# Kernel optimization log

Hardware: AMD Instinct MI355X
Metric: run time of the kernel (lower is better)

Reference implementation:

```python
import jax, jax.numpy as jnp
import numpy as np

DIM = 1024
HEADS = 16
EPS = 1e-05
B, T, C, H, W = 2, 16, DIM, 32, 32


def setup_inputs() -> dict:
    key = jax.random.key(0)
    ks = jax.random.split(key, 4)
    s = 1.0 / np.sqrt(DIM)
    return {
        "x": jax.random.normal(ks[0], (B, T, C, H, W), dtype=jnp.float32),
        "ln_w": jnp.ones((C,), dtype=jnp.float32),
        "ln_b": jnp.zeros((C,), dtype=jnp.float32),
        "Wq": jax.random.normal(ks[1], (C, C), dtype=jnp.float32) * s,
        "Wk": jax.random.normal(ks[2], (C, C), dtype=jnp.float32) * s,
        "Wv": jax.random.normal(ks[3], (C, C), dtype=jnp.float32) * s,
    }


def reference(x, ln_w, ln_b, Wq, Wk, Wv):
    b, t, c, h, w = x.shape
    heads = HEADS
    dh = c // heads
    scale = dh ** (-0.5)

    # Channel LayerNorm: normalize over C per (b,t,h,w)
    xc = jnp.transpose(x, (0, 1, 3, 4, 2))  # [B,T,H,W,C]
    mu = jnp.mean(xc, axis=-1, keepdims=True)
    var = jnp.mean(jnp.square(xc - mu), axis=-1, keepdims=True)
    xn = (xc - mu) * jax.lax.rsqrt(var + EPS) * ln_w + ln_b  # [B,T,H,W,C]

    # Q/K from spatial mean-pool
    pooled = jnp.mean(xn, axis=(2, 3))  # [B,T,C]
    q = pooled @ Wq.T  # [B,T,C]
    k = pooled @ Wk.T  # [B,T,C]

    # V per pixel; torch permutes to [B,W,H,T,C] then flattens W-major
    v = jnp.transpose(xn, (0, 3, 2, 1, 4)).reshape(b, h * w, t, c)  # [B,HW(w-major),T,C]
    v = v @ Wv.T

    q = q.reshape(b, t, heads, dh).transpose(0, 2, 1, 3) * scale  # [B,h,T,dh]
    k = k.reshape(b, t, heads, dh).transpose(0, 2, 3, 1)          # [B,h,dh,T]
    v = v.reshape(b, h * w, t, heads, dh).transpose(0, 1, 3, 2, 4)  # [B,HW,h,T,dh]

    attn = jax.nn.softmax(jnp.matmul(q, k), axis=-1)  # [B,h,T,T]
    out = jnp.einsum('bhst,bnhtd->bnhsd', attn, v)    # [B,HW,h,T,dh]
    # permute(0,3,2,4,1) -> [B,T,h,dh,HW], then view as (H,W)
    out = out.transpose(0, 3, 2, 4, 1).reshape(b, t, c, h, w)
    return out
```

## Files before the change

### kernel.cpp

```cpp
#include <hip/hip_runtime.h>
#include <stdint.h>
#include <stddef.h>

#define CDIM 1024
#define HWD  1024
#define TD   16
#define BD   2
#define NH   16
#define DHD  64

typedef __attribute__((ext_vector_type(8))) short bf16x8;
typedef __attribute__((ext_vector_type(4))) short bf16x4;
typedef __attribute__((ext_vector_type(4))) float f32x4;

static __device__ __forceinline__ short f2bf(float f) {
  uint32_t u = __builtin_bit_cast(uint32_t, f);
  uint32_t r = (u + 0x7FFFu + ((u >> 16) & 1u)) >> 16;
  return (short)(uint16_t)r;
}
static __device__ __forceinline__ float bf2f(short s) {
  return __builtin_bit_cast(float, (uint32_t)((uint16_t)s) << 16);
}

static __device__ __forceinline__ void gl_lds16(const short* g, short* l) {
  __builtin_amdgcn_global_load_lds((const __attribute__((address_space(1))) unsigned int*)g,
                                   (__attribute__((address_space(3))) unsigned int*)l,
                                   16, 0, 0);
}

__global__ void k_cast_w(const float* __restrict__ W, short* __restrict__ Wb) {
  int i = (blockIdx.x * 256 + threadIdx.x) * 4;
  f32x4 v = *(const f32x4*)&W[i];
  Wb[i + 0] = f2bf(v[0]);
  Wb[i + 1] = f2bf(v[1]);
  Wb[i + 2] = f2bf(v[2]);
  Wb[i + 3] = f2bf(v[3]);
}

__global__ __launch_bounds__(256) void k_ln_t(const float* __restrict__ x,
                                              const float* __restrict__ lnw,
                                              const float* __restrict__ lnb,
                                              short* __restrict__ xnT,
                                              float* __restrict__ part) {
  int bt = blockIdx.y;
  int p0 = blockIdx.x * 64;
  int tid = threadIdx.x;
  int pg = tid & 15, cs = tid >> 4;
  int pbase = p0 + pg * 4;
  const float* xs = x + (size_t)bt * CDIM * HWD;

  float s[4] = {}, s2[4] = {};
  #pragma unroll 8
  for (int j = 0; j < 64; ++j) {
    int c = cs + 16 * j;
    f32x4 v = *(const f32x4*)&xs[(size_t)c * HWD + pbase];
    #pragma unroll
    for (int i = 0; i < 4; ++i) { s[i] += v[i]; s2[i] += v[i] * v[i]; }
  }
  __shared__ float redA[16][64], redB[16][64];
  #pragma unroll
  for (int i = 0; i < 4; ++i) {
    redA[cs][pg * 4 + i] = s[i];
    redB[cs][pg * 4 + i] = s2[i];
  }
  __syncthreads();
  __shared__ float muS[64], rsS[64];
  if (tid < 64) {
    float a = 0.f, b2 = 0.f;
    #pragma unroll
    for (int k = 0; k < 16; ++k) { a += redA[k][tid]; b2 += redB[k][tid]; }
    float mu = a * (1.0f / CDIM);
    float var = b2 * (1.0f / CDIM) - mu * mu;
    muS[tid] = mu;
    rsS[tid] = rsqrtf(var + 1e-5f);
  }
  __syncthreads();
  float mu_[4], rs_[4];
  #pragma unroll
  for (int i = 0; i < 4; ++i) { mu_[i] = muS[pg * 4 + i]; rs_[i] = rsS[pg * 4 + i]; }

  __shared__ short tile[64 * 68];
  __shared__ float pr[64][17];
  short* outB = xnT + (size_t)bt * CDIM * HWD;

  for (int cb = 0; cb < 16; ++cb) {
    #pragma unroll
    for (int jj = 0; jj < 4; ++jj) {
      int cl = cs * 4 + jj;
      int c = cb * 64 + cl;
      f32x4 v = *(const f32x4*)&xs[(size_t)c * HWD + pbase];
      float w = lnw[c], bb = lnb[c];
      float psum = 0.f;
      #pragma unroll
      for (int i = 0; i < 4; ++i) {
        float xn = (v[i] - mu_[i]) * rs_[i] * w + bb;
        tile[(pg * 4 + i) * 68 + cl] = f2bf(xn);
        psum += xn;
      }
      pr[cl][pg] = psum;
    }
    __syncthreads();
    #pragma unroll
    for (int it = 0; it < 2; ++it) {
      int ch = it * 256 + tid;
      int plo = ch >> 3;
      int c8 = (ch & 7) * 8;
      bf16x4 a = *(const bf16x4*)&tile[plo * 68 + c8];
      bf16x4 b = *(const bf16x4*)&tile[plo * 68 + c8 + 4];
      int pq = p0 + plo;
      int q = (pq & 31) * 32 + (pq >> 5);
      short* dst = outB + (size_t)q * CDIM + cb * 64 + c8;
      *(bf16x4*)dst = a;
      *(bf16x4*)(dst + 4) = b;
    }
    if (tid < 64) {
      float a = 0.f;
      #pragma unroll
      for (int k = 0; k < 16; ++k) a += pr[tid][k];
      part[((size_t)bt * 16 + blockIdx.x) * CDIM + cb * 64 + tid] = a;
    }
    __syncthreads();
  }
}

__global__ void k_pool_red(const float* __restrict__ part, float* __restrict__ pooled,
                           short* __restrict__ pooledb) {
  int bt = blockIdx.y;
  int c = blockIdx.x * 256 + threadIdx.x;
  float s = 0.f;
  #pragma unroll
  for (int pc = 0; pc < 16; ++pc) s += part[((size_t)bt * 16 + pc) * CDIM + c];
  float m = s * (1.0f / HWD);
  pooled[bt * CDIM + c] = m;
  pooledb[bt * CDIM + c] = f2bf(m);
}

__global__ __launch_bounds__(256) void k_qk_mfma(const short* __restrict__ Wqkb,
                                                 const short* __restrict__ pooledb,
                                                 float* __restrict__ qm,
                                                 float* __restrict__ km) {
  int n0 = blockIdx.x * 128;
  __shared__ __align__(16) short lA[32 * 32];
  __shared__ __align__(16) short lB[128 * 32];
  int tid = threadIdx.x, lane = tid & 63, wid = tid >> 6;
  int s0 = wid * 128 + lane, s1 = s0 + 64;
  int fr = lane & 15, fk = (lane >> 4) * 8;
  f32x4 acc[2][2] = {};

  for (int kt = 0; kt < CDIM / 32; ++kt) {
    int k0 = kt * 32;
    __syncthreads();
    gl_lds16(&Wqkb[(size_t)(n0 + (s0 >> 2)) * CDIM + k0 + (s0 & 3) * 8], &lB[s0 * 8]);
    gl_lds16(&Wqkb[(size_t)(n0 + (s1 >> 2)) * CDIM + k0 + (s1 & 3) * 8], &lB[s1 * 8]);
    if (wid < 2) {
      gl_lds16(&pooledb[(size_t)(tid >> 2) * CDIM + k0 + (tid & 3) * 8], &lA[tid * 8]);
    }
    __syncthreads();
    bf16x8 af[2], bfr[2];
    #pragma unroll
    for (int mi = 0; mi < 2; ++mi)
      af[mi] = *(const bf16x8*)&lA[(mi * 16 + fr) * 32 + fk];
    #pragma unroll
    for (int ni = 0; ni < 2; ++ni)
      bfr[ni] = *(const bf16x8*)&lB[(wid * 32 + ni * 16 + fr) * 32 + fk];
    #pragma unroll
    for (int mi = 0; mi < 2; ++mi)
      #pragma unroll
      for (int ni = 0; ni < 2; ++ni)
        acc[mi][ni] = __builtin_amdgcn_mfma_f32_16x16x32_bf16(af[mi], bfr[ni], acc[mi][ni], 0, 0, 0);
  }

  int cr = lane >> 4;
  #pragma unroll
  for (int mi = 0; mi < 2; ++mi)
    #pragma unroll
    for (int ni = 0; ni < 2; ++ni)
      #pragma unroll
      for (int rr = 0; rr < 4; ++rr) {
        int row = mi * 16 + cr * 4 + rr;
        int col = n0 + wid * 32 + ni * 16 + fr;
        float v = acc[mi][ni][rr];
        if (col < 1024) qm[(size_t)row * CDIM + col] = v;
        else            km[(size_t)row * CDIM + col - 1024] = v;
      }
}

__global__ void k_attn(const float* __restrict__ qm, const float* __restrict__ km,
                       float* __restrict__ attn) {
  int bg = blockIdx.x;
  int b = bg >> 4, g = bg & 15;
  int s = threadIdx.x >> 4, t = threadIdx.x & 15;
  const float* qr = qm + (size_t)(b * TD + s) * CDIM + g * DHD;
  const float* kr = km + (size_t)(b * TD + t) * CDIM + g * DHD;
  float d = 0.f;
  #pragma unroll
  for (int i = 0; i < DHD; ++i) d += qr[i] * kr[i];
  d *= 0.125f;
  float m = d;
  #pragma unroll
  for (int off = 8; off; off >>= 1) m = fmaxf(m, __shfl_xor(m, off, 16));
  float e = __expf(d - m);
  float sum = e;
  #pragma unroll
  for (int off = 8; off; off >>= 1) sum += __shfl_xor(sum, off, 16);
  attn[(size_t)bg * 256 + s * 16 + t] = e / sum;
}

__global__ __launch_bounds__(512, 2) void k_vgemm(const short* __restrict__ Wb,
                                                  const short* __restrict__ xnT,
                                                  short* __restrict__ vp) {
  int bid = blockIdx.x;
  int swz = (bid & 7) * 64 + (bid >> 3);
  int bt = swz >> 4;
  int m0 = ((swz >> 2) & 3) * 256;
  int n0 = (swz & 3) * 256;
  const short* Bm = xnT + (size_t)bt * CDIM * HWD;

  __shared__ __align__(16) short lA[2][256 * 64];
  __shared__ __align__(16) short lB[2][256 * 64];

  int tid = threadIdx.x, lane = tid & 63, wid = tid >> 6;
  int wm = wid >> 2, wn = wid & 3;

  int srow = wid * 8 + (lane >> 3);
  int schunk = (lane & 7) ^ (lane >> 3);
  const short* gA = Wb + (size_t)(m0 + srow) * CDIM + schunk * 8;
  const short* gB = Bm + (size_t)(n0 + srow) * CDIM + schunk * 8;
  int doff = wid * 512 + lane * 8;

  int fr = lane & 15, klane = lane >> 4;
  int c0 = ((klane ^ (fr & 7)) * 8);
  int rA = (wm * 128 + fr) * 64;
  int rB = (wn * 64 + fr) * 64;

  f32x4 acc[8][4] = {};
  bf16x8 bq[4], af[4];

#define ISSUE(p, kt1, nb)                                                      \
  do {                                                                         \
    gl_lds16(gA + (size_t)(p) * 64 * CDIM + (kt1) * 64, &lA[nb][(p) * 4096 + doff]); \
    gl_lds16(gB + (size_t)(p) * 64 * CDIM + (kt1) * 64, &lB[nb][(p) * 4096 + doff]); \
  } while (0)
#define RDA(mi, ks, b) (*(const bf16x8*)&lA[b][rA + (mi) * 1024 + (c0 ^ ((ks) * 32))])
#define RDB(ni, ks, b) (*(const bf16x8*)&lB[b][rB + (ni) * 1024 + (c0 ^ ((ks) * 32))])

  ISSUE(0, 0, 0); ISSUE(1, 0, 0); ISSUE(2, 0, 0); ISSUE(3, 0, 0);

  for (int kt = 0; kt < 16; ++kt) {
    int cur = kt & 1, nxt = cur ^ 1;
    if (kt + 1 < 16) {
      ISSUE(0, kt + 1, nxt); ISSUE(1, kt + 1, nxt);
      ISSUE(2, kt + 1, nxt); ISSUE(3, kt + 1, nxt);
      asm volatile("s_waitcnt vmcnt(8)" ::: "memory");
    } else {
      asm volatile("s_waitcnt vmcnt(0)" ::: "memory");
    }
    __builtin_amdgcn_s_barrier();
    #pragma unroll
    for (int ni = 0; ni < 4; ++ni) bq[ni] = RDB(ni, 0, cur);
    #pragma unroll
    for (int mi = 0; mi < 4; ++mi) af[mi] = RDA(mi, 0, cur);
    __builtin_amdgcn_s_setprio(1);
    #pragma unroll
    for (int mi = 0; mi < 4; ++mi)
      #pragma unroll
      for (int ni = 0; ni < 4; ++ni)
        acc[mi][ni] = __builtin_amdgcn_mfma_f32_16x16x32_bf16(af[mi], bq[ni], acc[mi][ni], 0, 0, 0);
    __builtin_amdgcn_s_setprio(0);
    __builtin_amdgcn_s_barrier();
    #pragma unroll
    for (int mi = 0; mi < 4; ++mi) af[mi] = RDA(4 + mi, 0, cur);
    __builtin_amdgcn_s_barrier();
    __builtin_amdgcn_s_setprio(1);
    #pragma unroll
    for (int mi = 0; mi < 4; ++mi)
      #pragma unroll
      for (int ni = 0; ni < 4; ++ni)
        acc[4 + mi][ni] = __builtin_amdgcn_mfma_f32_16x16x32_bf16(af[mi], bq[ni], acc[4 + mi][ni], 0, 0, 0);
    __builtin_amdgcn_s_setprio(0);
    __builtin_amdgcn_s_barrier();
    #pragma unroll
    for (int ni = 0; ni < 4; ++ni) bq[ni] = RDB(ni, 1, cur);
    #pragma unroll
    for (int mi = 0; mi < 4; ++mi) af[mi] = RDA(mi, 1, cur);
    __builtin_amdgcn_s_barrier();
    __builtin_amdgcn_s_setprio(1);
    #pragma unroll
    for (int mi = 0; mi < 4; ++mi)
      #pragma unroll
      for (int ni = 0; ni < 4; ++ni)
        acc[mi][ni] = __builtin_amdgcn_mfma_f32_16x16x32_bf16(af[mi], bq[ni], acc[mi][ni], 0, 0, 0);
    __builtin_amdgcn_s_setprio(0);
    __builtin_amdgcn_s_barrier();
    #pragma unroll
    for (int mi = 0; mi < 4; ++mi) af[mi] = RDA(4 + mi, 1, cur);
    __builtin_amdgcn_s_barrier();
    __builtin_amdgcn_s_setprio(1);
    #pragma unroll
    for (int mi = 0; mi < 4; ++mi)
      #pragma unroll
      for (int ni = 0; ni < 4; ++ni)
        acc[4 + mi][ni] = __builtin_amdgcn_mfma_f32_16x16x32_bf16(af[mi], bq[ni], acc[4 + mi][ni], 0, 0, 0);
    __builtin_amdgcn_s_setprio(0);
    __builtin_amdgcn_s_barrier();
  }
#undef ISSUE
#undef RDA
#undef RDB

  short* outB = vp + (size_t)bt * CDIM * HWD;
  int cr = lane >> 4;
  #pragma unroll
  for (int mi = 0; mi < 8; ++mi)
    #pragma unroll
    for (int ni = 0; ni < 4; ++ni)
      #pragma unroll
      for (int r = 0; r < 4; ++r) {
        int row = m0 + wm * 128 + mi * 16 + cr * 4 + r;
        int col = n0 + wn * 64 + ni * 16 + fr;
        outB[(size_t)row * HWD + col] = f2bf(acc[mi][ni][r]);
      }
}

__global__ __launch_bounds__(256) void k_mix(const short* __restrict__ vp,
                                             const float* __restrict__ attn,
                                             float* __restrict__ out) {
  int c = blockIdx.x;
  int b = blockIdx.y;
  int g = c >> 6;
  __shared__ __align__(16) short vpl[TD * HWD];
  __shared__ float at[256];
  int tid = threadIdx.x;
  at[tid] = attn[(size_t)(b * NH + g) * 256 + tid];
  #pragma unroll
  for (int j = 0; j < 8; ++j) {
    int chunk = j * 256 + tid;
    int t = chunk >> 7, qc = chunk & 127;
    bf16x8 v = *(const bf16x8*)&vp[((size_t)(b * TD + t) * CDIM + c) * HWD + qc * 8];
    *(bf16x8*)&vpl[t * HWD + qc * 8] = v;
  }
  __syncthreads();
  int p = tid * 4;
  #pragma unroll
  for (int sh = 0; sh < 2; ++sh) {
    f32x4 acc[8] = {};
    #pragma unroll
    for (int t = 0; t < TD; ++t) {
      bf16x4 v4 = *(const bf16x4*)&vpl[t * HWD + p];
      f32x4 vf = {bf2f(v4[0]), bf2f(v4[1]), bf2f(v4[2]), bf2f(v4[3])};
      #pragma unroll
      for (int s8 = 0; s8 < 8; ++s8) {
        float a = at[(sh * 8 + s8) * 16 + t];
        acc[s8] += a * vf;
      }
    }
    #pragma unroll
    for (int s8 = 0; s8 < 8; ++s8) {
      int s = sh * 8 + s8;
      *(f32x4*)&out[((size_t)(b * TD + s) * CDIM + c) * HWD + p] = acc[s8];
    }
  }
}

extern "C" void kernel_launch(void* const* d_in, const int* in_sizes, int n_in,
                              void* d_out, int out_size, void* d_ws, size_t ws_size,
                              hipStream_t stream) {
  const float* x   = (const float*)d_in[0];
  const float* lnw = (const float*)d_in[1];
  const float* lnb = (const float*)d_in[2];
  const float* Wq  = (const float*)d_in[3];
  const float* Wk  = (const float*)d_in[4];
  const float* Wv  = (const float*)d_in[5];
  float* out = (float*)d_out;

  char* ws = (char*)d_ws;
  const size_t XNT_OFF   = 0;
  const size_t VP_OFF    = XNT_OFF + 67108864;
  const size_t WB_OFF    = VP_OFF + 67108864;
  const size_t WQKB_OFF  = WB_OFF + 2097152;
  const size_t POOLP_OFF = WQKB_OFF + 4194304;
  const size_t POOL_OFF  = POOLP_OFF + 2097152;
  const size_t POOLB_OFF = POOL_OFF + 131072;
  const size_t QM_OFF    = POOLB_OFF + 65536;
  const size_t KM_OFF    = QM_OFF + 131072;
  const size_t ATTN_OFF  = KM_OFF + 131072;

  short* xnT    = (short*)(ws + XNT_OFF);
  short* vp     = (short*)(ws + VP_OFF);
  short* Wb     = (short*)(ws + WB_OFF);
  short* Wqkb   = (short*)(ws + WQKB_OFF);
  float* poolp  = (float*)(ws + POOLP_OFF);
  float* pooled = (float*)(ws + POOL_OFF);
  short* poolb  = (short*)(ws + POOLB_OFF);
  float* qm     = (float*)(ws + QM_OFF);
  float* km     = (float*)(ws + KM_OFF);
  float* attn   = (float*)(ws + ATTN_OFF);

  k_cast_w<<<dim3(1024), 256, 0, stream>>>(Wv, Wb);
  k_cast_w<<<dim3(1024), 256, 0, stream>>>(Wq, Wqkb);
  k_cast_w<<<dim3(1024), 256, 0, stream>>>(Wk, Wqkb + 1048576);
  k_ln_t<<<dim3(16, 32), 256, 0, stream>>>(x, lnw, lnb, xnT, poolp);
  k_pool_red<<<dim3(4, 32), 256, 0, stream>>>(poolp, pooled, poolb);
  k_qk_mfma<<<dim3(16), 256, 0, stream>>>(Wqkb, poolb, qm, km);
  k_attn<<<dim3(32), 256, 0, stream>>>(qm, km, attn);
  k_vgemm<<<dim3(512), 512, 0, stream>>>(Wb, xnT, vp);
  k_mix<<<dim3(1024, 2), 256, 0, stream>>>(vp, attn, out);
}
```

Measured before the change: 231.4 us.

## Triple-buffer V GEMM with 32-wide K tiles and shrink LayerNorm tiles

The V-projection GEMM moves from double-buffered 64-wide K tiles to triple-buffered 32-wide K tiles. The second half of each next-tile load is issued in the middle of the compute step, and the LDS swizzle is adjusted to match, so global loads overlap MFMA work more deeply. The LayerNorm/transpose kernel now processes 16 pixels per block instead of 64, giving four times as many blocks and 16-byte transposed stores. Pooled partial sums are stored in the not-yet-used vp buffer and the unused fp32 pooled output is dropped. The trade-offs are more barriers per K step in the GEMM, and four times more partial sums for the pool reduction to read.

```diff
diff --git a/kernel.cpp b/kernel.cpp
--- a/kernel.cpp
+++ b/kernel.cpp
@@ -43,32 +43,31 @@
                                               short* __restrict__ xnT,
                                               float* __restrict__ part) {
   int bt = blockIdx.y;
-  int p0 = blockIdx.x * 64;
+  int p0 = blockIdx.x * 16;
   int tid = threadIdx.x;
-  int pg = tid & 15, cs = tid >> 4;
+  int pg = tid & 3, cs = tid >> 2;
   int pbase = p0 + pg * 4;
   const float* xs = x + (size_t)bt * CDIM * HWD;
 
   float s[4] = {}, s2[4] = {};
-  #pragma unroll 8
-  for (int j = 0; j < 64; ++j) {
-    int c = cs + 16 * j;
+  #pragma unroll
+  for (int j = 0; j < 16; ++j) {
+    int c = cs + 64 * j;
     f32x4 v = *(const f32x4*)&xs[(size_t)c * HWD + pbase];
     #pragma unroll
     for (int i = 0; i < 4; ++i) { s[i] += v[i]; s2[i] += v[i] * v[i]; }
   }
-  __shared__ float redA[16][64], redB[16][64];
+  __shared__ float redA[64][16], redB[64][16];
   #pragma unroll
   for (int i = 0; i < 4; ++i) {
     redA[cs][pg * 4 + i] = s[i];
     redB[cs][pg * 4 + i] = s2[i];
   }
   __syncthreads();
-  __shared__ float muS[64], rsS[64];
-  if (tid < 64) {
+  __shared__ float muS[16], rsS[16];
+  if (tid < 16) {
     float a = 0.f, b2 = 0.f;
-    #pragma unroll
-    for (int k = 0; k < 16; ++k) { a += redA[k][tid]; b2 += redB[k][tid]; }
+    for (int k = 0; k < 64; ++k) { a += redA[k][tid]; b2 += redB[k][tid]; }
     float mu = a * (1.0f / CDIM);
     float var = b2 * (1.0f / CDIM) - mu * mu;
     muS[tid] = mu;
@@ -79,22 +78,22 @@
   #pragma unroll
   for (int i = 0; i < 4; ++i) { mu_[i] = muS[pg * 4 + i]; rs_[i] = rsS[pg * 4 + i]; }
 
-  __shared__ short tile[64 * 68];
-  __shared__ float pr[64][17];
+  __shared__ short tile[16 * 272];
+  __shared__ float pr[256][4];
   short* outB = xnT + (size_t)bt * CDIM * HWD;
 
-  for (int cb = 0; cb < 16; ++cb) {
+  for (int cb = 0; cb < 4; ++cb) {
     #pragma unroll
     for (int jj = 0; jj < 4; ++jj) {
       int cl = cs * 4 + jj;
-      int c = cb * 64 + cl;
+      int c = cb * 256 + cl;
       f32x4 v = *(const f32x4*)&xs[(size_t)c * HWD + pbase];
       float w = lnw[c], bb = lnb[c];
       float psum = 0.f;
       #pragma unroll
       for (int i = 0; i < 4; ++i) {
         float xn = (v[i] - mu_[i]) * rs_[i] * w + bb;
-        tile[(pg * 4 + i) * 68 + cl] = f2bf(xn);
+        tile[(pg * 4 + i) * 272 + cl] = f2bf(xn);
         psum += xn;
       }
       pr[cl][pg] = psum;
@@ -103,36 +102,28 @@
     #pragma unroll
     for (int it = 0; it < 2; ++it) {
       int ch = it * 256 + tid;
-      int plo = ch >> 3;
-      int c8 = (ch & 7) * 8;
-      bf16x4 a = *(const bf16x4*)&tile[plo * 68 + c8];
-      bf16x4 b = *(const bf16x4*)&tile[plo * 68 + c8 + 4];
+      int plo = ch >> 5;
+      int c8 = (ch & 31) * 8;
+      bf16x8 vv = *(const bf16x8*)&tile[plo * 272 + c8];
       int pq = p0 + plo;
       int q = (pq & 31) * 32 + (pq >> 5);
-      short* dst = outB + (size_t)q * CDIM + cb * 64 + c8;
-      *(bf16x4*)dst = a;
-      *(bf16x4*)(dst + 4) = b;
-    }
-    if (tid < 64) {
-      float a = 0.f;
-      #pragma unroll
-      for (int k = 0; k < 16; ++k) a += pr[tid][k];
-      part[((size_t)bt * 16 + blockIdx.x) * CDIM + cb * 64 + tid] = a;
+      *(bf16x8*)&outB[(size_t)q * CDIM + cb * 256 + c8] = vv;
+    }
+    {
+      float a = pr[tid][0] + pr[tid][1] + pr[tid][2] + pr[tid][3];
+      part[((size_t)bt * 64 + blockIdx.x) * CDIM + cb * 256 + tid] = a;
     }
     __syncthreads();
   }
 }
 
-__global__ void k_pool_red(const float* __restrict__ part, float* __restrict__ pooled,
-                           short* __restrict__ pooledb) {
+__global__ void k_pool_red(const float* __restrict__ part, short* __restrict__ pooledb) {
   int bt = blockIdx.y;
   int c = blockIdx.x * 256 + threadIdx.x;
   float s = 0.f;
   #pragma unroll
-  for (int pc = 0; pc < 16; ++pc) s += part[((size_t)bt * 16 + pc) * CDIM + c];
-  float m = s * (1.0f / HWD);
-  pooled[bt * CDIM + c] = m;
-  pooledb[bt * CDIM + c] = f2bf(m);
+  for (int pc = 0; pc < 64; ++pc) s += part[((size_t)bt * 64 + pc) * CDIM + c];
+  pooledb[bt * CDIM + c] = f2bf(s * (1.0f / HWD));
 }
 
 __global__ __launch_bounds__(256) void k_qk_mfma(const short* __restrict__ Wqkb,
@@ -209,6 +200,7 @@
 __global__ __launch_bounds__(512, 2) void k_vgemm(const short* __restrict__ Wb,
                                                   const short* __restrict__ xnT,
                                                   short* __restrict__ vp) {
+  const int NT = CDIM / 32;
   int bid = blockIdx.x;
   int swz = (bid & 7) * 64 + (bid >> 3);
   int bt = swz >> 4;
@@ -216,50 +208,49 @@
   int n0 = (swz & 3) * 256;
   const short* Bm = xnT + (size_t)bt * CDIM * HWD;
 
-  __shared__ __align__(16) short lA[2][256 * 64];
-  __shared__ __align__(16) short lB[2][256 * 64];
-
-  int tid = threadIdx.x, lane = tid & 63, wid = tid >> 6;
-  int wm = wid >> 2, wn = wid & 3;
-
-  int srow = wid * 8 + (lane >> 3);
-  int schunk = (lane & 7) ^ (lane >> 3);
-  const short* gA = Wb + (size_t)(m0 + srow) * CDIM + schunk * 8;
-  const short* gB = Bm + (size_t)(n0 + srow) * CDIM + schunk * 8;
-  int doff = wid * 512 + lane * 8;
-
-  int fr = lane & 15, klane = lane >> 4;
-  int c0 = ((klane ^ (fr & 7)) * 8);
-  int rA = (wm * 128 + fr) * 64;
-  int rB = (wn * 64 + fr) * 64;
+  __shared__ __align__(16) short lA[3][256 * 32];
+  __shared__ __align__(16) short lB[3][256 * 32];
+
+  int tid = threadIdx.x, l = tid & 63, w = tid >> 6;
+  int wm = w >> 2, wn = w & 3;
+
+  int rowoff = w * 16 + (l >> 2);
+  int lc8 = ((l & 3) ^ ((l >> 3) & 3)) * 8;
+  const short* gA = Wb + (size_t)(m0 + rowoff) * CDIM + lc8;
+  const short* gB = Bm + (size_t)(n0 + rowoff) * CDIM + lc8;
+  int ldsoff = (w * 64 + l) * 8;
+
+  int fr = l & 15, klane = l >> 4;
+  int c0 = (klane ^ ((fr >> 1) & 3)) * 8;
+  int rA = (wm * 128 + fr) * 32;
+  int rB = (wn * 64 + fr) * 32;
 
   f32x4 acc[8][4] = {};
   bf16x8 bq[4], af[4];
 
-#define ISSUE(p, kt1, nb)                                                      \
-  do {                                                                         \
-    gl_lds16(gA + (size_t)(p) * 64 * CDIM + (kt1) * 64, &lA[nb][(p) * 4096 + doff]); \
-    gl_lds16(gB + (size_t)(p) * 64 * CDIM + (kt1) * 64, &lB[nb][(p) * 4096 + doff]); \
+#define ISSUE(g, kt2, bf)                                                          \
+  do {                                                                             \
+    gl_lds16(gA + (size_t)(g) * 128 * CDIM + (kt2) * 32, &lA[bf][(g) * 4096 + ldsoff]); \
+    gl_lds16(gB + (size_t)(g) * 128 * CDIM + (kt2) * 32, &lB[bf][(g) * 4096 + ldsoff]); \
   } while (0)
-#define RDA(mi, ks, b) (*(const bf16x8*)&lA[b][rA + (mi) * 1024 + (c0 ^ ((ks) * 32))])
-#define RDB(ni, ks, b) (*(const bf16x8*)&lB[b][rB + (ni) * 1024 + (c0 ^ ((ks) * 32))])
-
-  ISSUE(0, 0, 0); ISSUE(1, 0, 0); ISSUE(2, 0, 0); ISSUE(3, 0, 0);
-
-  for (int kt = 0; kt < 16; ++kt) {
-    int cur = kt & 1, nxt = cur ^ 1;
-    if (kt + 1 < 16) {
-      ISSUE(0, kt + 1, nxt); ISSUE(1, kt + 1, nxt);
-      ISSUE(2, kt + 1, nxt); ISSUE(3, kt + 1, nxt);
-      asm volatile("s_waitcnt vmcnt(8)" ::: "memory");
-    } else {
-      asm volatile("s_waitcnt vmcnt(0)" ::: "memory");
-    }
+#define RDA(mi, bf) (*(const bf16x8*)&lA[bf][rA + (mi) * 512 + c0])
+#define RDB(ni, bf) (*(const bf16x8*)&lB[bf][rB + (ni) * 512 + c0])
+
+  ISSUE(0, 0, 0); ISSUE(1, 0, 0);
+  ISSUE(0, 1, 1); ISSUE(1, 1, 1);
+
+  for (int kt = 0; kt < NT; ++kt) {
+    int cb = kt % 3;
+    int pb = (kt + 2) % 3;
+    if (kt + 2 < NT) ISSUE(0, kt + 2, pb);
+    if (kt < NT - 2)       asm volatile("s_waitcnt vmcnt(6)" ::: "memory");
+    else if (kt == NT - 2) asm volatile("s_waitcnt vmcnt(4)" ::: "memory");
+    else                   asm volatile("s_waitcnt vmcnt(0)" ::: "memory");
     __builtin_amdgcn_s_barrier();
     #pragma unroll
-    for (int ni = 0; ni < 4; ++ni) bq[ni] = RDB(ni, 0, cur);
-    #pragma unroll
-    for (int mi = 0; mi < 4; ++mi) af[mi] = RDA(mi, 0, cur);
+    for (int ni = 0; ni < 4; ++ni) bq[ni] = RDB(ni, cb);
+    #pragma unroll
+    for (int mi = 0; mi < 4; ++mi) af[mi] = RDA(mi, cb);
     __builtin_amdgcn_s_setprio(1);
     #pragma unroll
     for (int mi = 0; mi < 4; ++mi)
@@ -268,8 +259,9 @@
         acc[mi][ni] = __builtin_amdgcn_mfma_f32_16x16x32_bf16(af[mi], bq[ni], acc[mi][ni], 0, 0, 0);
     __builtin_amdgcn_s_setprio(0);
     __builtin_amdgcn_s_barrier();
-    #pragma unroll
-    for (int mi = 0; mi < 4; ++mi) af[mi] = RDA(4 + mi, 0, cur);
+    if (kt + 2 < NT) ISSUE(1, kt + 2, pb);
+    #pragma unroll
+    for (int mi = 0; mi < 4; ++mi) af[mi] = RDA(4 + mi, cb);
     __builtin_amdgcn_s_barrier();
     __builtin_amdgcn_s_setprio(1);
     #pragma unroll
@@ -279,37 +271,13 @@
         acc[4 + mi][ni] = __builtin_amdgcn_mfma_f32_16x16x32_bf16(af[mi], bq[ni], acc[4 + mi][ni], 0, 0, 0);
     __builtin_amdgcn_s_setprio(0);
     __builtin_amdgcn_s_barrier();
-    #pragma unroll
-    for (int ni = 0; ni < 4; ++ni) bq[ni] = RDB(ni, 1, cur);
-    #pragma unroll
-    for (int mi = 0; mi < 4; ++mi) af[mi] = RDA(mi, 1, cur);
-    __builtin_amdgcn_s_barrier();
-    __builtin_amdgcn_s_setprio(1);
-    #pragma unroll
-    for (int mi = 0; mi < 4; ++mi)
-      #pragma unroll
-      for (int ni = 0; ni < 4; ++ni)
-        acc[mi][ni] = __builtin_amdgcn_mfma_f32_16x16x32_bf16(af[mi], bq[ni], acc[mi][ni], 0, 0, 0);
-    __builtin_amdgcn_s_setprio(0);
-    __builtin_amdgcn_s_barrier();
-    #pragma unroll
-    for (int mi = 0; mi < 4; ++mi) af[mi] = RDA(4 + mi, 1, cur);
-    __builtin_amdgcn_s_barrier();
-    __builtin_amdgcn_s_setprio(1);
-    #pragma unroll
-    for (int mi = 0; mi < 4; ++mi)
-      #pragma unroll
-      for (int ni = 0; ni < 4; ++ni)
-        acc[4 + mi][ni] = __builtin_amdgcn_mfma_f32_16x16x32_bf16(af[mi], bq[ni], acc[4 + mi][ni], 0, 0, 0);
-    __builtin_amdgcn_s_setprio(0);
-    __builtin_amdgcn_s_barrier();
   }
 #undef ISSUE
 #undef RDA
 #undef RDB
 
   short* outB = vp + (size_t)bt * CDIM * HWD;
-  int cr = lane >> 4;
+  int cr = l >> 4;
   #pragma unroll
   for (int mi = 0; mi < 8; ++mi)
     #pragma unroll
@@ -378,19 +346,16 @@
   const size_t VP_OFF    = XNT_OFF + 67108864;
   const size_t WB_OFF    = VP_OFF + 67108864;
   const size_t WQKB_OFF  = WB_OFF + 2097152;
-  const size_t POOLP_OFF = WQKB_OFF + 4194304;
-  const size_t POOL_OFF  = POOLP_OFF + 2097152;
-  const size_t POOLB_OFF = POOL_OFF + 131072;
+  const size_t POOLB_OFF = WQKB_OFF + 4194304;
   const size_t QM_OFF    = POOLB_OFF + 65536;
   const size_t KM_OFF    = QM_OFF + 131072;
   const size_t ATTN_OFF  = KM_OFF + 131072;
 
   short* xnT    = (short*)(ws + XNT_OFF);
   short* vp     = (short*)(ws + VP_OFF);
+  float* poolp  = (float*)(ws + VP_OFF);
   short* Wb     = (short*)(ws + WB_OFF);
   short* Wqkb   = (short*)(ws + WQKB_OFF);
-  float* poolp  = (float*)(ws + POOLP_OFF);
-  float* pooled = (float*)(ws + POOL_OFF);
   short* poolb  = (short*)(ws + POOLB_OFF);
   float* qm     = (float*)(ws + QM_OFF);
   float* km     = (float*)(ws + KM_OFF);
@@ -399,8 +364,8 @@
   k_cast_w<<<dim3(1024), 256, 0, stream>>>(Wv, Wb);
   k_cast_w<<<dim3(1024), 256, 0, stream>>>(Wq, Wqkb);
   k_cast_w<<<dim3(1024), 256, 0, stream>>>(Wk, Wqkb + 1048576);
-  k_ln_t<<<dim3(16, 32), 256, 0, stream>>>(x, lnw, lnb, xnT, poolp);
-  k_pool_red<<<dim3(4, 32), 256, 0, stream>>>(poolp, pooled, poolb);
+  k_ln_t<<<dim3(64, 32), 256, 0, stream>>>(x, lnw, lnb, xnT, poolp);
+  k_pool_red<<<dim3(4, 32), 256, 0, stream>>>(poolp, poolb);
   k_qk_mfma<<<dim3(16), 256, 0, stream>>>(Wqkb, poolb, qm, km);
   k_attn<<<dim3(32), 256, 0, stream>>>(qm, km, attn);
   k_vgemm<<<dim3(512), 512, 0, stream>>>(Wb, xnT, vp);
```

After: 277.1 us. 1.2x slower.
